# Optimization experiments

Hardware: AMD Instinct MI355X
Metric: run time of the kernel (lower is better)

The kernel has to match this reference:

```python
import jax, jax.numpy as jnp
import numpy as np
from jax import lax

DIM = 32       # MemoryLayerAttention dim
HEADS = 4      # MemoryLayerAttention heads
R = 2 * HEADS * DIM   # cell memory_rows = 256
C = DIM               # cell memory_columns = 32
E = 32         # cell embedding_size (default)
CH = 4         # cell MHA heads (default)
KD = 32        # keras MHA key_dim = embedding_size
FF = 128       # cell feed_forward_size (default)
EPS = 1e-6     # LayerNormalization epsilon


def _pos_encoding(length, d):
    # standard sinusoidal positional encoding, shape (1, length, d)
    pos = np.arange(length)[:, None].astype(np.float32)
    i = np.arange(d)[None, :]
    angle = pos / np.power(10000.0, (2 * (i // 2)) / d)
    pe = np.where(i % 2 == 0, np.sin(angle), np.cos(angle)).astype(np.float32)
    return jnp.asarray(pe)[None]


def setup_inputs():
    key = jax.random.key(0)
    ks = jax.random.split(key, 16)
    def w(k, shape):
        return jax.random.normal(k, shape, jnp.float32) * 0.05
    return {
        "queries": jax.random.normal(ks[0], (32, 4, DIM), jnp.float32),
        "values": jax.random.normal(ks[1], (32, 8, DIM), jnp.float32),
        "W_in": w(ks[2], (2 * DIM, E)), "b_in": jnp.zeros((E,), jnp.float32),
        "W_me": w(ks[3], (C, E)), "b_me": jnp.zeros((E,), jnp.float32),
        "Wq": w(ks[4], (E, CH, KD)), "bq": jnp.zeros((CH, KD), jnp.float32),
        "Wk": w(ks[5], (E, CH, KD)), "bk": jnp.zeros((CH, KD), jnp.float32),
        "Wv": w(ks[6], (E, CH, KD)), "bv": jnp.zeros((CH, KD), jnp.float32),
        "Wo": w(ks[7], (CH, KD, E)), "bo": jnp.zeros((E,), jnp.float32),
        "W_f1": w(ks[8], (E, FF)), "b_f1": jnp.zeros((FF,), jnp.float32),
        "W_f2": w(ks[9], (FF, E)), "b_f2": jnp.zeros((E,), jnp.float32),
        "ln_g": jnp.ones((E,), jnp.float32), "ln_b": jnp.zeros((E,), jnp.float32),
        "W_out": w(ks[10], (E, 1)), "b_out": jnp.zeros((1,), jnp.float32),
        "W_mi": w(ks[11], (E, 1 + C)), "b_mi": jnp.zeros((1 + C,), jnp.float32),
    }


def _ln(x, g, b):
    m = jnp.mean(x, -1, keepdims=True)
    v = jnp.mean((x - m) ** 2, -1, keepdims=True)
    return (x - m) / jnp.sqrt(v + EPS) * g + b


def _forward(queries, values, W_in, b_in, W_me, b_me, Wq, bq, Wk, bk, Wv, bv,
             Wo, bo, W_f1, b_f1, W_f2, b_f2, ln_g, ln_b, W_out, b_out, W_mi, b_mi):
    B, Q, D = queries.shape
    V = values.shape[1]
    # cross-pair every query with every value -> RNN batch of size B*Q, seq len V
    dq = jnp.repeat(queries[:, :, None, :], V, 2)          # (B, Q, V, D)
    dv = jnp.repeat(values[:, None, :, :], Q, 1)           # (B, Q, V, D)
    x = jnp.concatenate([dq, dv], -1).reshape(B * Q, V, 2 * D)  # (N, V, 2D)
    N = B * Q
    pe = _pos_encoding(1 + R, E)                           # (1, 1+R, E)
    scale = 1.0 / float(np.sqrt(KD))

    def mha(z):  # keras MultiHeadAttention(CH heads, key_dim=KD), self-attn on (N, L, E)
        q = jnp.einsum('nle,ehk->nlhk', z, Wq) + bq
        k = jnp.einsum('nle,ehk->nlhk', z, Wk) + bk
        v = jnp.einsum('nle,ehk->nlhk', z, Wv) + bv
        s = jnp.einsum('nqhk,nlhk->nhql', q, k) * scale    # (N, H, L, L)
        a = jax.nn.softmax(s, -1)
        o = jnp.einsum('nhql,nlhk->nqhk', a, v)
        return jnp.einsum('nqhk,hke->nqe', o, Wo) + bo

    def step(mem, inp):  # mem: (N, R, C), inp: (N, 2D)
        em = mem @ W_me + b_me                             # (N, R, E)
        ei = (inp @ W_in + b_in)[:, None, :]               # (N, 1, E)
        aug = jnp.concatenate([ei, em], 1) + pe            # (N, 1+R, E)
        att = _ln(mha(aug) + aug, ln_g, ln_b)
        h = jnp.maximum(att @ W_f1 + b_f1, 0.0) @ W_f2 + b_f2 + att
        nf = _ln(h, ln_g, ln_b)
        out = nf[:, 0, :] @ W_out + b_out                  # (N, 1)
        mi = nf[:, 1:, :] @ W_mi + b_mi                    # (N, R, 1+C)
        cs = jax.nn.sigmoid(mi[..., :1])                   # double sigmoid, as in source
        mem = jax.nn.sigmoid(-cs) * mem + jax.nn.sigmoid(cs) * mi[..., 1:]
        return mem, out

    mem0 = jnp.full((N, R, C), 1e-6, jnp.float32)
    _, outs = lax.scan(step, mem0, jnp.swapaxes(x, 0, 1))  # outs: (V, N, 1)
    # keras RNN (no return_sequences) keeps only the last step's output
    return outs[-1].reshape(-1, Q, D)


def reference(queries, values, W_in, b_in, W_me, b_me, Wq, bq, Wk, bk, Wv, bv,
              Wo, bo, W_f1, b_f1, W_f2, b_f2, ln_g, ln_b, W_out, b_out, W_mi, b_mi):
    return _forward(queries, values, W_in, b_in, W_me, b_me, Wq, bq, Wk, bk, Wv, bv,
                    Wo, bo, W_f1, b_f1, W_f2, b_f2, ln_g, ln_b, W_out, b_out, W_mi, b_mi)
```

## Files before the change

### kernel.cpp

```cpp
#include <hip/hip_runtime.h>
#include <math.h>


#define L_SEQ 257
#define SCALE 0.17677669529663689f

#define MEM_SZ  (128*256*32)
#define Z_SZ    (128*257*32)
#define HO_SZ   (128*4*257*32)
#define NF_SZ   (128*257*32)
#define PE_SZ   (L_SEQ*32)
#define QKV_SZ  (512*L_SEQ*32)

__global__ void k_init(float* __restrict__ mem) {
  const int i = blockIdx.x*256 + threadIdx.x;
  if (i < MEM_SZ) mem[i] = 1e-6f;
}

__global__ void k_pe(float* __restrict__ pe) {
  const int i = blockIdx.x*256 + threadIdx.x;
  if (i >= L_SEQ*32) return;
  const int row = i >> 5, e = i & 31;
  const int k = e >> 1;
  const double p10 = pow(10000.0, (double)(2*k)/32.0);
  const double ang = (double)row / p10;
  pe[i] = (float)((e & 1) ? cos(ang) : sin(ang));
}

__global__ __launch_bounds__(256, 2)
void k_aug(const float* __restrict__ queries, const float* __restrict__ values,
           const float* __restrict__ W_in, const float* __restrict__ b_in,
           const float* __restrict__ W_me, const float* __restrict__ b_me,
           const float* __restrict__ mem, const float* __restrict__ pe,
           float* __restrict__ z, int t) {
  const int gid = blockIdx.x*256 + threadIdx.x;
  if (gid >= 128*L_SEQ) return;
  const int e0 = blockIdx.y * 8;
  const int n = gid / L_SEQ, row = gid - n*L_SEQ;
  float acc[8];
  if (row == 0) {
    #pragma unroll
    for (int k = 0; k < 8; k++) acc[k] = b_in[e0+k];
    const float* q = queries + n*32;
    const float* v = values + (size_t)((n>>2)*8 + t)*32;
    for (int c = 0; c < 32; c++) {
      const float qc = q[c], vc = v[c];
      #pragma unroll
      for (int k = 0; k < 8; k++) acc[k] += qc*W_in[c*32+e0+k] + vc*W_in[(32+c)*32+e0+k];
    }
  } else {
    #pragma unroll
    for (int k = 0; k < 8; k++) acc[k] = b_me[e0+k];
    const float* mr = mem + ((size_t)n*256 + (row-1))*32;
    for (int c = 0; c < 32; c++) {
      const float mc = mr[c];
      #pragma unroll
      for (int k = 0; k < 8; k++) acc[k] += mc*W_me[c*32+e0+k];
    }
  }
  float* zr = z + (size_t)gid*32 + e0;
  const float* per = pe + row*32 + e0;
  #pragma unroll
  for (int k = 0; k < 8; k++) zr[k] = acc[k] + per[k];
}

__global__ __launch_bounds__(256, 2)
void k_proj(const float* __restrict__ z,
            const float* __restrict__ Wq, const float* __restrict__ bq,
            const float* __restrict__ Wk, const float* __restrict__ bk,
            const float* __restrict__ Wv, const float* __restrict__ bv,
            float* __restrict__ Kg, float* __restrict__ Vg,
            float* __restrict__ Qg) {
  const int nh = blockIdx.x, which = blockIdx.y;
  const int n = nh >> 2, h = nh & 3;
  const float* W  = (which == 0) ? Wk : (which == 1) ? Wv : Wq;
  const float* bb = (which == 0) ? bk : (which == 1) ? bv : bq;
  float* out      = (which == 0) ? Kg : (which == 1) ? Vg : Qg;
  const float scale = (which == 2) ? SCALE : 1.0f;
  const float* zb = z + (size_t)n*L_SEQ*32;

  for (int r = threadIdx.x; r < L_SEQ; r += 256) {
    float acc[32];
    #pragma unroll
    for (int d = 0; d < 32; d++) acc[d] = bb[h*32+d];
    const float4* z4 = (const float4*)(zb + r*32);
    #pragma unroll 2
    for (int c8 = 0; c8 < 8; c8++) {
      const float4 zc = z4[c8];
      const float zv[4] = {zc.x, zc.y, zc.z, zc.w};
      #pragma unroll
      for (int q = 0; q < 4; q++) {
        const int e = c8*4 + q;
        const float ze = zv[q];
        #pragma unroll
        for (int d = 0; d < 32; d++) acc[d] += ze * W[e*128 + h*32 + d];
      }
    }
    float4* dst = (float4*)(out + ((size_t)nh*L_SEQ + r)*32);
    #pragma unroll
    for (int c = 0; c < 8; c++)
      dst[c] = make_float4(acc[4*c]*scale, acc[4*c+1]*scale, acc[4*c+2]*scale, acc[4*c+3]*scale);
  }
}

__global__ __launch_bounds__(256, 4)
void k_attn(const float* __restrict__ Qg, const float* __restrict__ Kg,
            const float* __restrict__ Vg, const float* __restrict__ Wo,
            float* __restrict__ headout) {
  __shared__ float pbuf[3][64][35];
  const int nh = blockIdx.x, rg = blockIdx.y;
  const int h = nh & 3;
  const int tid = threadIdx.x;
  const int wave = __builtin_amdgcn_readfirstlane(tid >> 6);
  const int lane = tid & 63;
  const int row = rg*64 + lane;
  const float* Kb = Kg + (size_t)nh*L_SEQ*32;
  const float* Vb = Vg + (size_t)nh*L_SEQ*32;
  const float* Qb = Qg + (size_t)nh*L_SEQ*32;
  const float* wo = Wo + h*1024;
  float* hob = headout + (size_t)nh*L_SEQ*32;

  float q[32];
  {
    const float4* qr = (const float4*)(Qb + (size_t)row*32);
    #pragma unroll
    for (int c = 0; c < 8; c++) {
      const float4 t4 = qr[c];
      q[4*c] = t4.x; q[4*c+1] = t4.y; q[4*c+2] = t4.z; q[4*c+3] = t4.w;
    }
  }
  float o[32];
  #pragma unroll
  for (int d = 0; d < 32; d++) o[d] = 0.f;
  float m = -1e30f, sum = 0.f;
  const int l0 = wave*64;

  #pragma unroll 1
  for (int ch = 0; ch < 8; ch++) {
    float sc[8];
    #pragma unroll
    for (int jj = 0; jj < 8; jj++) {
      const int l = l0 + ch*8 + jj;
      const float4* kr = (const float4*)(Kb + l*32);
      float s0 = 0.f, s1 = 0.f, s2 = 0.f, s3 = 0.f;
      #pragma unroll
      for (int c = 0; c < 8; c++) {
        const float4 kc = kr[c];
        s0 += q[4*c]*kc.x;   s1 += q[4*c+1]*kc.y;
        s2 += q[4*c+2]*kc.z; s3 += q[4*c+3]*kc.w;
      }
      sc[jj] = (s0 + s1) + (s2 + s3);
    }
    float cm = sc[0];
    #pragma unroll
    for (int jj = 1; jj < 8; jj++) cm = fmaxf(cm, sc[jj]);
    if (!__all(cm <= m)) {
      const float nm = fmaxf(m, cm);
      const float e0 = __expf(m - nm);
      sum *= e0;
      #pragma unroll
      for (int d = 0; d < 32; d++) o[d] *= e0;
      m = nm;
    }
    #pragma unroll
    for (int jj = 0; jj < 8; jj++) {
      const int l = l0 + ch*8 + jj;
      const float p = __expf(sc[jj] - m);
      sum += p;
      const float4* vr = (const float4*)(Vb + l*32);
      #pragma unroll
      for (int c = 0; c < 8; c++) {
        const float4 vc = vr[c];
        o[4*c]   += p*vc.x; o[4*c+1] += p*vc.y;
        o[4*c+2] += p*vc.z; o[4*c+3] += p*vc.w;
      }
    }
  }
  if (wave == 3) {
    const float4* kr = (const float4*)(Kb + 256*32);
    float s0 = 0.f, s1 = 0.f, s2 = 0.f, s3 = 0.f;
    #pragma unroll
    for (int c = 0; c < 8; c++) {
      const float4 kc = kr[c];
      s0 += q[4*c]*kc.x;   s1 += q[4*c+1]*kc.y;
      s2 += q[4*c+2]*kc.z; s3 += q[4*c+3]*kc.w;
    }
    const float x = (s0 + s1) + (s2 + s3);
    const float nm = fmaxf(m, x);
    const float e0 = __expf(m - nm), p = __expf(x - nm);
    sum = sum*e0 + p;
    const float4* vr = (const float4*)(Vb + 256*32);
    #pragma unroll
    for (int c = 0; c < 8; c++) {
      const float4 vc = vr[c];
      o[4*c]   = o[4*c]*e0   + p*vc.x; o[4*c+1] = o[4*c+1]*e0 + p*vc.y;
      o[4*c+2] = o[4*c+2]*e0 + p*vc.z; o[4*c+3] = o[4*c+3]*e0 + p*vc.w;
    }
    m = nm;
  }
  if (wave > 0) {
    pbuf[wave-1][lane][0] = m;
    pbuf[wave-1][lane][1] = sum;
    #pragma unroll
    for (int c = 0; c < 32; c++) pbuf[wave-1][lane][2+c] = o[c];
  }
  __syncthreads();
  if (wave == 0) {
    #pragma unroll 1
    for (int w = 0; w < 3; w++) {
      const float mw = pbuf[w][lane][0];
      const float sw = pbuf[w][lane][1];
      const float nm = fmaxf(m, mw);
      const float f = __expf(m - nm), g = __expf(mw - nm);
      sum = sum*f + sw*g;
      #pragma unroll
      for (int c = 0; c < 32; c++) o[c] = o[c]*f + g*pbuf[w][lane][2+c];
      m = nm;
    }
    const float inv = 1.f/sum;
    float outv[32];
    #pragma unroll 4
    for (int d = 0; d < 32; d++) {
      float a = 0.f;
      #pragma unroll
      for (int kd = 0; kd < 32; kd++) a += o[kd]*wo[kd*32 + d];
      outv[d] = a*inv;
    }
    float4* dst = (float4*)(hob + (size_t)row*32);
    #pragma unroll
    for (int c = 0; c < 8; c++)
      dst[c] = make_float4(outv[4*c], outv[4*c+1], outv[4*c+2], outv[4*c+3]);
  }

  if (rg == 3) {
    float q2[32];
    {
      const float4* qr = (const float4*)(Qb + 256*32);
      #pragma unroll
      for (int c = 0; c < 8; c++) {
        const float4 t4 = qr[c];
        q2[4*c] = t4.x; q2[4*c+1] = t4.y; q2[4*c+2] = t4.z; q2[4*c+3] = t4.w;
      }
    }
    float m2, s2, o2[32];
    {
      const int l = l0 + lane;
      const float4* kr = (const float4*)(Kb + l*32);
      const float4* vr = (const float4*)(Vb + l*32);
      float s0 = 0.f, s1 = 0.f, sp = 0.f, s3 = 0.f;
      #pragma unroll
      for (int c = 0; c < 8; c++) {
        const float4 kc = kr[c];
        s0 += q2[4*c]*kc.x;   s1 += q2[4*c+1]*kc.y;
        sp += q2[4*c+2]*kc.z; s3 += q2[4*c+3]*kc.w;
      }
      m2 = (s0 + s1) + (sp + s3);
      s2 = 1.f;
      #pragma unroll
      for (int c = 0; c < 8; c++) {
        const float4 vc = vr[c];
        o2[4*c] = vc.x; o2[4*c+1] = vc.y; o2[4*c+2] = vc.z; o2[4*c+3] = vc.w;
      }
    }
    if (wave == 3 && lane == 0) {
      const float4* kr = (const float4*)(Kb + 256*32);
      const float4* vr = (const float4*)(Vb + 256*32);
      float s0 = 0.f, s1 = 0.f, sp = 0.f, s3 = 0.f;
      #pragma unroll
      for (int c = 0; c < 8; c++) {
        const float4 kc = kr[c];
        s0 += q2[4*c]*kc.x;   s1 += q2[4*c+1]*kc.y;
        sp += q2[4*c+2]*kc.z; s3 += q2[4*c+3]*kc.w;
      }
      const float x = (s0 + s1) + (sp + s3);
      const float nm = fmaxf(m2, x);
      const float e0 = __expf(m2 - nm), p = __expf(x - nm);
      s2 = s2*e0 + p;
      #pragma unroll
      for (int c = 0; c < 8; c++) {
        const float4 vc = vr[c];
        o2[4*c]   = o2[4*c]*e0   + p*vc.x; o2[4*c+1] = o2[4*c+1]*e0 + p*vc.y;
        o2[4*c+2] = o2[4*c+2]*e0 + p*vc.z; o2[4*c+3] = o2[4*c+3]*e0 + p*vc.w;
      }
      m2 = nm;
    }
    #pragma unroll 1
    for (int off = 1; off < 64; off <<= 1) {
      const float om = __shfl_xor(m2, off);
      const float os = __shfl_xor(s2, off);
      const float nm = fmaxf(m2, om);
      const float me = __expf(m2 - nm), oe = __expf(om - nm);
      s2 = s2*me + os*oe;
      #pragma unroll
      for (int d = 0; d < 32; d++) o2[d] = o2[d]*me + __shfl_xor(o2[d], off)*oe;
      m2 = nm;
    }
    __syncthreads();
    if (lane == 0) {
      pbuf[0][wave][0] = m2;
      pbuf[0][wave][1] = s2;
      #pragma unroll
      for (int c = 0; c < 32; c++) pbuf[0][wave][2+c] = o2[c];
    }
    __syncthreads();
    if (wave == 0) {
      float mw[4], fw[4];
      #pragma unroll
      for (int w = 0; w < 4; w++) mw[w] = pbuf[0][w][0];
      float M = fmaxf(fmaxf(mw[0], mw[1]), fmaxf(mw[2], mw[3]));
      float S = 0.f;
      #pragma unroll
      for (int w = 0; w < 4; w++) {
        fw[w] = __expf(mw[w] - M);
        S += pbuf[0][w][1]*fw[w];
      }
      const int c = lane & 31;
      float om = 0.f;
      #pragma unroll
      for (int w = 0; w < 4; w++) om += fw[w]*pbuf[0][w][2+c];
      float a = 0.f;
      #pragma unroll
      for (int kd = 0; kd < 32; kd++) a += __shfl(om, kd) * wo[kd*32 + c];
      if (lane < 32) hob[256*32 + c] = a / S;
    }
  }
}

__global__ __launch_bounds__(256, 2)
void k_ffln(const float* __restrict__ headout, const float* __restrict__ z,
            const float* __restrict__ bo,
            const float* __restrict__ W_f1, const float* __restrict__ b_f1,
            const float* __restrict__ W_f2, const float* __restrict__ b_f2,
            const float* __restrict__ ln_g, const float* __restrict__ ln_b,
            const float* __restrict__ W_out, const float* __restrict__ b_out,
            float* __restrict__ nf, float* __restrict__ outp, int t) {
  __shared__ float ybuf[3][64][33];
  const int tid = threadIdx.x;
  const int wave = __builtin_amdgcn_readfirstlane(tid >> 6);
  const int lane = tid & 63;
  const int rowid = blockIdx.x*64 + lane;
  const int n = rowid / L_SEQ, row = rowid - n*L_SEQ;

  float att[32];
  const float* hob = headout + (size_t)n*4*L_SEQ*32 + (size_t)row*32;
  const float* zr = z + (size_t)rowid*32;
  #pragma unroll
  for (int e = 0; e < 32; e++)
    att[e] = bo[e] + zr[e] + hob[e] + hob[L_SEQ*32 + e]
           + hob[2*L_SEQ*32 + e] + hob[3*L_SEQ*32 + e];
  float mu = 0.f;
  #pragma unroll
  for (int e = 0; e < 32; e++) mu += att[e];
  mu *= (1.f/32.f);
  float var = 0.f;
  #pragma unroll
  for (int e = 0; e < 32; e++) { const float d = att[e]-mu; var += d*d; }
  var *= (1.f/32.f);
  float rstd = 1.f/sqrtf(var + 1e-6f);
  #pragma unroll
  for (int e = 0; e < 32; e++) att[e] = (att[e]-mu)*rstd*ln_g[e] + ln_b[e];

  float y[32];
  #pragma unroll
  for (int e = 0; e < 32; e++) y[e] = 0.f;
  const int j0 = wave*32;
  #pragma unroll 1
  for (int jj = 0; jj < 32; jj++) {
    const int j = j0 + jj;
    float hv = b_f1[j];
    #pragma unroll
    for (int e = 0; e < 32; e++) hv += att[e]*W_f1[e*128 + j];
    hv = fmaxf(hv, 0.f);
    #pragma unroll
    for (int e = 0; e < 32; e++) y[e] += hv*W_f2[j*32 + e];
  }
  if (wave > 0) {
    #pragma unroll
    for (int e = 0; e < 32; e++) ybuf[wave-1][lane][e] = y[e];
  }
  __syncthreads();
  if (wave > 0) return;

  #pragma unroll
  for (int e = 0; e < 32; e++)
    y[e] += ybuf[0][lane][e] + ybuf[1][lane][e] + ybuf[2][lane][e]
          + b_f2[e] + att[e];

  mu = 0.f;
  #pragma unroll
  for (int e = 0; e < 32; e++) mu += y[e];
  mu *= (1.f/32.f);
  var = 0.f;
  #pragma unroll
  for (int e = 0; e < 32; e++) { const float d = y[e]-mu; var += d*d; }
  var *= (1.f/32.f);
  rstd = 1.f/sqrtf(var + 1e-6f);
  float nfv[32];
  #pragma unroll
  for (int e = 0; e < 32; e++) nfv[e] = (y[e]-mu)*rstd*ln_g[e] + ln_b[e];

  float4* nr = (float4*)(nf + (size_t)rowid*32);
  #pragma unroll
  for (int c = 0; c < 8; c++)
    nr[c] = make_float4(nfv[4*c], nfv[4*c+1], nfv[4*c+2], nfv[4*c+3]);

  if (t == 7 && row == 0) {
    float a = b_out[0];
    #pragma unroll
    for (int e = 0; e < 32; e++) a += nfv[e]*W_out[e];
    outp[n] = a;
  }
}

__global__ __launch_bounds__(256, 2)
void k_memaug(const float* __restrict__ queries, const float* __restrict__ values,
              const float* __restrict__ W_in, const float* __restrict__ b_in,
              const float* __restrict__ W_me, const float* __restrict__ b_me,
              const float* __restrict__ W_mi, const float* __restrict__ b_mi,
              const float* __restrict__ nf, const float* __restrict__ pe,
              float* __restrict__ mem, float* __restrict__ z, int tnext) {
  const int gid = blockIdx.x*256 + threadIdx.x;
  if (gid >= 128*L_SEQ) return;
  const int n = gid / L_SEQ, row = gid - n*L_SEQ;
  float acc[32];
  if (row == 0) {
    #pragma unroll
    for (int e = 0; e < 32; e++) acc[e] = b_in[e];
    const float* q = queries + n*32;
    const float* v = values + (size_t)((n>>2)*8 + tnext)*32;
    for (int c = 0; c < 32; c++) {
      const float qc = q[c], vc = v[c];
      #pragma unroll
      for (int e = 0; e < 32; e++) acc[e] += qc*W_in[c*32+e] + vc*W_in[(32+c)*32+e];
    }
  } else {
    float xr[32];
    const float* x = nf + (size_t)gid*32;
    #pragma unroll
    for (int e = 0; e < 32; e++) xr[e] = x[e];
    float mi0 = b_mi[0];
    #pragma unroll
    for (int e = 0; e < 32; e++) mi0 += xr[e]*W_mi[e*33];
    const float cs = 1.f/(1.f + expf(-mi0));
    const float ga = 1.f/(1.f + expf(cs));
    const float gb = 1.f/(1.f + expf(-cs));
    float* mr = mem + ((size_t)n*256 + (row-1))*32;
    float mnew[32];
    #pragma unroll 1
    for (int c = 0; c < 32; c++) {
      float mic = b_mi[1+c];
      #pragma unroll
      for (int e = 0; e < 32; e++) mic += xr[e]*W_mi[e*33 + 1 + c];
      mnew[c] = ga*mr[c] + gb*mic;
    }
    #pragma unroll
    for (int c = 0; c < 8; c++)
      ((float4*)mr)[c] = make_float4(mnew[4*c], mnew[4*c+1], mnew[4*c+2], mnew[4*c+3]);
    #pragma unroll
    for (int e = 0; e < 32; e++) acc[e] = b_me[e];
    for (int c = 0; c < 32; c++) {
      const float mc = mnew[c];
      #pragma unroll
      for (int e = 0; e < 32; e++) acc[e] += mc*W_me[c*32+e];
    }
  }
  const float* per = pe + row*32;
  float4* zr = (float4*)(z + (size_t)gid*32);
  #pragma unroll
  for (int c = 0; c < 8; c++)
    zr[c] = make_float4(acc[4*c]+per[4*c], acc[4*c+1]+per[4*c+1],
                        acc[4*c+2]+per[4*c+2], acc[4*c+3]+per[4*c+3]);
}

extern "C" void kernel_launch(void* const* d_in, const int* in_sizes, int n_in,
                              void* d_out, int out_size, void* d_ws, size_t ws_size,
                              hipStream_t stream) {
  const float* queries = (const float*)d_in[0];
  const float* values  = (const float*)d_in[1];
  const float* W_in = (const float*)d_in[2];   const float* b_in = (const float*)d_in[3];
  const float* W_me = (const float*)d_in[4];   const float* b_me = (const float*)d_in[5];
  const float* Wq   = (const float*)d_in[6];   const float* bq   = (const float*)d_in[7];
  const float* Wk   = (const float*)d_in[8];   const float* bk   = (const float*)d_in[9];
  const float* Wv   = (const float*)d_in[10];  const float* bv   = (const float*)d_in[11];
  const float* Wo   = (const float*)d_in[12];  const float* bo   = (const float*)d_in[13];
  const float* W_f1 = (const float*)d_in[14];  const float* b_f1 = (const float*)d_in[15];
  const float* W_f2 = (const float*)d_in[16];  const float* b_f2 = (const float*)d_in[17];
  const float* ln_g = (const float*)d_in[18];  const float* ln_b = (const float*)d_in[19];
  const float* W_out= (const float*)d_in[20];  const float* b_out= (const float*)d_in[21];
  const float* W_mi = (const float*)d_in[22];  const float* b_mi = (const float*)d_in[23];

  float* ws  = (float*)d_ws;
  float* mem = ws;
  float* z   = mem + MEM_SZ;
  float* ho  = z   + Z_SZ;
  float* nf  = ho  + HO_SZ;
  float* pe  = nf  + NF_SZ;
  float* Kg  = pe  + PE_SZ;
  float* Vg  = Kg  + QKV_SZ;
  float* Qg  = Vg  + QKV_SZ;
  float* outp = (float*)d_out;

  k_init<<<MEM_SZ/256, 256, 0, stream>>>(mem);
  k_pe<<<(L_SEQ*32 + 255)/256, 256, 0, stream>>>(pe);
  k_aug<<<dim3(129, 4), 256, 0, stream>>>(queries, values, W_in, b_in,
                                          W_me, b_me, mem, pe, z, 0);
  for (int t = 0; t < 8; t++) {
    k_proj<<<dim3(512, 3), 256, 0, stream>>>(z, Wq, bq, Wk, bk, Wv, bv, Kg, Vg, Qg);
    k_attn<<<dim3(512, 4), 256, 0, stream>>>(Qg, Kg, Vg, Wo, ho);
    k_ffln<<<514, 256, 0, stream>>>(ho, z, bo, W_f1, b_f1, W_f2, b_f2,
                                    ln_g, ln_b, W_out, b_out, nf, outp, t);
    if (t < 7)
      k_memaug<<<129, 256, 0, stream>>>(queries, values, W_in, b_in, W_me, b_me,
                                        W_mi, b_mi, nf, pe, mem, z, t+1);
  }
}
```

Before: 1.953 ms.

## Split per-row output projections across all four waves in attention, FFN and memory update

The attention epilogue no longer has wave 0 alone do the 32x32 Wo projection. The merged softmax state is staged in shared memory and each wave computes 8 output columns. In the FFN/LN kernel all four waves now redundantly perform the final reduction and layernorm, with each writing one quarter of the row. The memory-update kernel moves from one thread per row to four waves per row group (4x more blocks), each handling 8 columns and sharing the new memory row through LDS. Launch bounds are raised and the score loop is unrolled by 2, trading redundant work and extra barriers for more parallelism on the serial tails.

Measured after the change: 1.751 ms. -10.3%, faster.

```diff
diff --git a/kernel.cpp b/kernel.cpp
--- a/kernel.cpp
+++ b/kernel.cpp
@@ -135,7 +135,7 @@
   float m = -1e30f, sum = 0.f;
   const int l0 = wave*64;
 
-  #pragma unroll 1
+  #pragma unroll 2
   for (int ch = 0; ch < 8; ch++) {
     float sc[8];
     #pragma unroll
@@ -217,19 +217,28 @@
       for (int c = 0; c < 32; c++) o[c] = o[c]*f + g*pbuf[w][lane][2+c];
       m = nm;
     }
-    const float inv = 1.f/sum;
-    float outv[32];
-    #pragma unroll 4
-    for (int d = 0; d < 32; d++) {
+    pbuf[0][lane][0] = 1.f/sum;
+    #pragma unroll
+    for (int c = 0; c < 32; c++) pbuf[0][lane][2+c] = o[c];
+  }
+  __syncthreads();
+  {
+    const float inv = pbuf[0][lane][0];
+    float oc[32];
+    #pragma unroll
+    for (int c = 0; c < 32; c++) oc[c] = pbuf[0][lane][2+c];
+    const int d0 = wave*8;
+    float outv[8];
+    #pragma unroll
+    for (int dd = 0; dd < 8; dd++) {
       float a = 0.f;
       #pragma unroll
-      for (int kd = 0; kd < 32; kd++) a += o[kd]*wo[kd*32 + d];
-      outv[d] = a*inv;
-    }
-    float4* dst = (float4*)(hob + (size_t)row*32);
-    #pragma unroll
-    for (int c = 0; c < 8; c++)
-      dst[c] = make_float4(outv[4*c], outv[4*c+1], outv[4*c+2], outv[4*c+3]);
+      for (int kd = 0; kd < 32; kd++) a += oc[kd]*wo[kd*32 + d0 + dd];
+      outv[dd] = a*inv;
+    }
+    float4* dst = (float4*)(hob + (size_t)row*32 + d0);
+    dst[0] = make_float4(outv[0], outv[1], outv[2], outv[3]);
+    dst[1] = make_float4(outv[4], outv[5], outv[6], outv[7]);
   }
 
   if (rg == 3) {
@@ -326,7 +335,7 @@
   }
 }
 
-__global__ __launch_bounds__(256, 2)
+__global__ __launch_bounds__(256, 4)
 void k_ffln(const float* __restrict__ headout, const float* __restrict__ z,
             const float* __restrict__ bo,
             const float* __restrict__ W_f1, const float* __restrict__ b_f1,
@@ -334,7 +343,7 @@
             const float* __restrict__ ln_g, const float* __restrict__ ln_b,
             const float* __restrict__ W_out, const float* __restrict__ b_out,
             float* __restrict__ nf, float* __restrict__ outp, int t) {
-  __shared__ float ybuf[3][64][33];
+  __shared__ float ybuf[4][64][33];
   const int tid = threadIdx.x;
   const int wave = __builtin_amdgcn_readfirstlane(tid >> 6);
   const int lane = tid & 63;
@@ -374,17 +383,14 @@
     #pragma unroll
     for (int e = 0; e < 32; e++) y[e] += hv*W_f2[j*32 + e];
   }
-  if (wave > 0) {
-    #pragma unroll
-    for (int e = 0; e < 32; e++) ybuf[wave-1][lane][e] = y[e];
-  }
+  #pragma unroll
+  for (int e = 0; e < 32; e++) ybuf[wave][lane][e] = y[e];
   __syncthreads();
-  if (wave > 0) return;
 
   #pragma unroll
   for (int e = 0; e < 32; e++)
-    y[e] += ybuf[0][lane][e] + ybuf[1][lane][e] + ybuf[2][lane][e]
-          + b_f2[e] + att[e];
+    y[e] = ybuf[0][lane][e] + ybuf[1][lane][e] + ybuf[2][lane][e]
+         + ybuf[3][lane][e] + b_f2[e] + att[e];
 
   mu = 0.f;
   #pragma unroll
@@ -399,12 +405,11 @@
   #pragma unroll
   for (int e = 0; e < 32; e++) nfv[e] = (y[e]-mu)*rstd*ln_g[e] + ln_b[e];
 
-  float4* nr = (float4*)(nf + (size_t)rowid*32);
-  #pragma unroll
-  for (int c = 0; c < 8; c++)
-    nr[c] = make_float4(nfv[4*c], nfv[4*c+1], nfv[4*c+2], nfv[4*c+3]);
-
-  if (t == 7 && row == 0) {
+  float4* nr = (float4*)(nf + (size_t)rowid*32 + wave*8);
+  nr[0] = make_float4(nfv[wave*8+0], nfv[wave*8+1], nfv[wave*8+2], nfv[wave*8+3]);
+  nr[1] = make_float4(nfv[wave*8+4], nfv[wave*8+5], nfv[wave*8+6], nfv[wave*8+7]);
+
+  if (t == 7 && row == 0 && wave == 0) {
     float a = b_out[0];
     #pragma unroll
     for (int e = 0; e < 32; e++) a += nfv[e]*W_out[e];
@@ -412,64 +417,78 @@
   }
 }
 
-__global__ __launch_bounds__(256, 2)
+__global__ __launch_bounds__(256, 4)
 void k_memaug(const float* __restrict__ queries, const float* __restrict__ values,
               const float* __restrict__ W_in, const float* __restrict__ b_in,
               const float* __restrict__ W_me, const float* __restrict__ b_me,
               const float* __restrict__ W_mi, const float* __restrict__ b_mi,
               const float* __restrict__ nf, const float* __restrict__ pe,
               float* __restrict__ mem, float* __restrict__ z, int tnext) {
-  const int gid = blockIdx.x*256 + threadIdx.x;
-  if (gid >= 128*L_SEQ) return;
-  const int n = gid / L_SEQ, row = gid - n*L_SEQ;
-  float acc[32];
-  if (row == 0) {
-    #pragma unroll
-    for (int e = 0; e < 32; e++) acc[e] = b_in[e];
+  __shared__ float mbuf[64][33];
+  const int tid = threadIdx.x;
+  const int wave = __builtin_amdgcn_readfirstlane(tid >> 6);
+  const int lane = tid & 63;
+  const int rowid = blockIdx.x*64 + lane;
+  const int n = rowid / L_SEQ, row = rowid - n*L_SEQ;
+  const int e0 = wave*8;
+  const bool isrow0 = (row == 0);
+
+  if (!isrow0) {
+    float xr[32];
+    const float4* x4 = (const float4*)(nf + (size_t)rowid*32);
+    #pragma unroll
+    for (int c = 0; c < 8; c++) {
+      const float4 t4 = x4[c];
+      xr[4*c] = t4.x; xr[4*c+1] = t4.y; xr[4*c+2] = t4.z; xr[4*c+3] = t4.w;
+    }
+    float mi0 = b_mi[0];
+    #pragma unroll
+    for (int e = 0; e < 32; e++) mi0 += xr[e]*W_mi[e*33];
+    const float cs = 1.f/(1.f + expf(-mi0));
+    const float ga = 1.f/(1.f + expf(cs));
+    const float gb = 1.f/(1.f + expf(-cs));
+    float* mr = mem + ((size_t)n*256 + (row-1))*32 + e0;
+    float mnew[8];
+    #pragma unroll
+    for (int cc = 0; cc < 8; cc++) {
+      const int c = e0 + cc;
+      float mic = b_mi[1+c];
+      #pragma unroll
+      for (int e = 0; e < 32; e++) mic += xr[e]*W_mi[e*33 + 1 + c];
+      mnew[cc] = ga*mr[cc] + gb*mic;
+    }
+    ((float4*)mr)[0] = make_float4(mnew[0], mnew[1], mnew[2], mnew[3]);
+    ((float4*)mr)[1] = make_float4(mnew[4], mnew[5], mnew[6], mnew[7]);
+    #pragma unroll
+    for (int cc = 0; cc < 8; cc++) mbuf[lane][e0+cc] = mnew[cc];
+  }
+  __syncthreads();
+
+  float acc[8];
+  if (isrow0) {
+    #pragma unroll
+    for (int k = 0; k < 8; k++) acc[k] = b_in[e0+k];
     const float* q = queries + n*32;
     const float* v = values + (size_t)((n>>2)*8 + tnext)*32;
     for (int c = 0; c < 32; c++) {
       const float qc = q[c], vc = v[c];
       #pragma unroll
-      for (int e = 0; e < 32; e++) acc[e] += qc*W_in[c*32+e] + vc*W_in[(32+c)*32+e];
+      for (int k = 0; k < 8; k++) acc[k] += qc*W_in[c*32+e0+k] + vc*W_in[(32+c)*32+e0+k];
     }
   } else {
-    float xr[32];
-    const float* x = nf + (size_t)gid*32;
-    #pragma unroll
-    for (int e = 0; e < 32; e++) xr[e] = x[e];
-    float mi0 = b_mi[0];
-    #pragma unroll
-    for (int e = 0; e < 32; e++) mi0 += xr[e]*W_mi[e*33];
-    const float cs = 1.f/(1.f + expf(-mi0));
-    const float ga = 1.f/(1.f + expf(cs));
-    const float gb = 1.f/(1.f + expf(-cs));
-    float* mr = mem + ((size_t)n*256 + (row-1))*32;
-    float mnew[32];
-    #pragma unroll 1
+    #pragma unroll
+    for (int k = 0; k < 8; k++) acc[k] = b_me[e0+k];
+    #pragma unroll 4
     for (int c = 0; c < 32; c++) {
-      float mic = b_mi[1+c];
-      #pragma unroll
-      for (int e = 0; e < 32; e++) mic += xr[e]*W_mi[e*33 + 1 + c];
-      mnew[c] = ga*mr[c] + gb*mic;
-    }
-    #pragma unroll
-    for (int c = 0; c < 8; c++)
-      ((float4*)mr)[c] = make_float4(mnew[4*c], mnew[4*c+1], mnew[4*c+2], mnew[4*c+3]);
-    #pragma unroll
-    for (int e = 0; e < 32; e++) acc[e] = b_me[e];
-    for (int c = 0; c < 32; c++) {
-      const float mc = mnew[c];
-      #pragma unroll
-      for (int e = 0; e < 32; e++) acc[e] += mc*W_me[c*32+e];
-    }
-  }
-  const float* per = pe + row*32;
-  float4* zr = (float4*)(z + (size_t)gid*32);
-  #pragma unroll
-  for (int c = 0; c < 8; c++)
-    zr[c] = make_float4(acc[4*c]+per[4*c], acc[4*c+1]+per[4*c+1],
-                        acc[4*c+2]+per[4*c+2], acc[4*c+3]+per[4*c+3]);
+      const float mc = mbuf[lane][c];
+      #pragma unroll
+      for (int k = 0; k < 8; k++) acc[k] += mc*W_me[c*32+e0+k];
+    }
+  }
+  const float* per = pe + row*32 + e0;
+  float4* zr = (float4*)(z + (size_t)rowid*32 + e0);
+  zr[0] = make_float4(acc[0]+per[0], acc[1]+per[1], acc[2]+per[2], acc[3]+per[3]);
+  zr[1] = make_float4(acc[4]+per[4], acc[5]+per[5], acc[6]+per[6], acc[7]+per[7]);
 }
 
 extern "C" void kernel_launch(void* const* d_in, const int* in_sizes, int n_in,
@@ -510,7 +529,7 @@
     k_ffln<<<514, 256, 0, stream>>>(ho, z, bo, W_f1, b_f1, W_f2, b_f2,
                                     ln_g, ln_b, W_out, b_out, nf, outp, t);
     if (t < 7)
-      k_memaug<<<129, 256, 0, stream>>>(queries, values, W_in, b_in, W_me, b_me,
+      k_memaug<<<514, 256, 0, stream>>>(queries, values, W_in, b_in, W_me, b_me,
                                         W_mi, b_mi, nf, pe, mem, z, t+1);
   }
 }
```
